# Kernel tuning notes

Measured on AMD Instinct MI355X. Metric: run time of the kernel, lower is better.

## Reference

```python
import jax, jax.numpy as jnp
import numpy as np

DIM = 16
BOND = 4
RANK = 512
N = 50000
E = 400000
F_IN = 16
EDGE_VARIABLE = 2


def setup_inputs() -> dict:
    key = jax.random.key(0)
    ks = iter(jax.random.split(key, 48))
    g = lambda shape, s=0.1: jax.random.normal(next(ks), shape, jnp.float32) * s
    inp = {
        "x": jax.random.normal(next(ks), (N, F_IN), jnp.float32),
        "node_type": jax.random.randint(next(ks), (N,), 0, 3),
        "edge_index": jax.random.randint(next(ks), (2, E), 0, N),
        "edge_attr": jax.random.uniform(next(ks), (E, BOND), dtype=jnp.float32),
        # lin0
        "W_lin0": g((F_IN, DIM)), "b_lin0": jnp.zeros((DIM,), jnp.float32),
        # NNConv: root weight + edge-conditioned weight MLP (4 -> 32 -> dim*dim)
        "W_root": g((DIM, DIM)), "b_conv": jnp.zeros((DIM,), jnp.float32),
        "W_e1": g((BOND, 32)), "b_e1": jnp.zeros((32,), jnp.float32),
        "W_e2": g((32, DIM * DIM)), "b_e2": jnp.zeros((DIM * DIM,), jnp.float32),
        # GRU (torch gate order r,z,n), weights stored torch-style [3*dim, dim]
        "W_ih": g((3 * DIM, DIM)), "b_ih": jnp.zeros((3 * DIM,), jnp.float32),
        "W_hh": g((3 * DIM, DIM)), "b_hh": jnp.zeros((3 * DIM,), jnp.float32),
        # projections
        "W_lin1": g((DIM, BOND)), "b_lin1": jnp.zeros((BOND,), jnp.float32),
        "W_up": g((BOND, DIM)), "b_up": jnp.zeros((DIM,), jnp.float32),
        "W_down": g((DIM, BOND)), "b_down": jnp.zeros((BOND,), jnp.float32),
        # FGNet low-rank factor modules (rank 512)
        "U_B": g((DIM, RANK)), "V_B": g((RANK, DIM)),
        "U_C": g((DIM, RANK)), "V_C": g((RANK, DIM)),
        "U_A": g((BOND, RANK)), "V_A": g((RANK, BOND)),
        # fusion weights
        "w_node": g((1, DIM)), "W_lin": g((DIM, DIM)), "b_lin": jnp.zeros((DIM,), jnp.float32),
        "w_edge": g((1, BOND)), "W_line": g((BOND, BOND)), "b_line": jnp.zeros((BOND,), jnp.float32),
    }
    return inp


def _forward(x, edge_attr, W_lin0, b_lin0, W_root, b_conv, W_e1, b_e1, W_e2, b_e2,
             W_ih, b_ih, W_hh, b_hh, W_lin1, b_lin1, W_up, b_up, W_down, b_down,
             U_B, V_B, U_C, V_C, U_A, V_A, w_node, W_lin, b_lin, w_edge, W_line, b_line,
             node_type, edge_index):
    src, dst = edge_index[0], edge_index[1]

    def nnconv(out):
        # per-edge weight matrices from edge features (edge-conditioned conv)
        he = jax.nn.relu(edge_attr @ W_e1 + b_e1)
        We = (he @ W_e2 + b_e2).reshape(E, DIM, DIM)          # [E, dim, dim]
        m = jnp.einsum('ed,edk->ek', out[src], We)             # gather-multiply
        agg = jax.ops.segment_sum(m, dst, num_segments=N)      # scatter-add
        deg = jax.ops.segment_sum(jnp.ones((E,), out.dtype), dst, num_segments=N)
        agg = agg / jnp.clip(deg, 1.0)[:, None]                # mean aggregation
        return out @ W_root + b_conv + agg

    def gru(inp, h):
        gi = inp @ W_ih.T + b_ih
        gh = h @ W_hh.T + b_hh
        i_r, i_z, i_n = jnp.split(gi, 3, axis=-1)
        h_r, h_z, h_n = jnp.split(gh, 3, axis=-1)
        r = jax.nn.sigmoid(i_r + h_r)
        z = jax.nn.sigmoid(i_z + h_z)
        n = jnp.tanh(i_n + r * h_n)
        return (1.0 - z) * n + z * h

    out = jax.nn.relu(x @ W_lin0 + b_lin0)                     # [N, dim]
    h = out
    for _ in range(3):
        m = jax.nn.relu(nnconv(out))
        h = gru(m, h)
        out = h

    out_edges = jax.nn.relu(out @ W_lin1 + b_lin1)             # [N, bond]

    # one outer message-passing round (k in range(1))
    ev_mask = (node_type == EDGE_VARIABLE)[:, None]
    out_edges_up = out_edges @ W_up + b_up                     # [N, dim]
    out_combine = jnp.where(ev_mask, out_edges_up, out)        # masked replace

    # factor-B message (low-rank FGNet) -> node-dim message + down-projected edge msg
    msg_B = jax.nn.relu((out_combine @ U_B) @ V_B)             # [N, dim]
    msg_to_edge_B = msg_B @ W_down + b_down                    # [N, bond]

    # factor-C message (low-rank FGNet)
    msg_C = jax.nn.relu((out_combine @ U_C) @ V_C)             # [N, dim]

    # factor-A / valence message on edge-type beliefs
    msg_to_edge_A = jax.nn.relu((out_edges @ U_A) @ V_A)       # [N, bond]

    all_msg = msg_B + msg_C                                    # sum over stacked msgs
    combine_edge_msg = msg_to_edge_A * msg_to_edge_B

    out = out + jax.nn.relu((w_node * all_msg) @ W_lin + b_lin)
    out_edges = out_edges + jax.nn.relu((w_edge * combine_edge_msg) @ W_line + b_line)

    return jax.nn.log_softmax(out_edges, axis=-1)              # [N, bond]


def reference(x, node_type, edge_index, edge_attr, W_lin0, b_lin0, W_root, b_conv,
              W_e1, b_e1, W_e2, b_e2, W_ih, b_ih, W_hh, b_hh, W_lin1, b_lin1,
              W_up, b_up, W_down, b_down, U_B, V_B, U_C, V_C, U_A, V_A,
              w_node, W_lin, b_lin, w_edge, W_line, b_line):
    return _forward(x, edge_attr, W_lin0, b_lin0, W_root, b_conv, W_e1, b_e1, W_e2, b_e2,
                    W_ih, b_ih, W_hh, b_hh, W_lin1, b_lin1, W_up, b_up, W_down, b_down,
                    U_B, V_B, U_C, V_C, U_A, V_A, w_node, W_lin, b_lin, w_edge, W_line, b_line,
                    node_type, edge_index)
```

## Files before the change

kernel.cpp:

```cpp
#include <hip/hip_runtime.h>
#include <hip/hip_bf16.h>
#include <math.h>

#define N_NODES 50000
#define N_EDGES 400000
#define DIM 16
#define BOND 4
#define NCHUNK 25000
#define EDGE_GRID 784
#define E_BLOCKS 1563
#define PRE_BASE (E_BLOCKS - 68)
#define SCAN_TILE 1024
#define SCAN_BLOCKS 49

typedef __attribute__((ext_vector_type(8))) short short8;
typedef __attribute__((ext_vector_type(4))) float f32x4;

__device__ __forceinline__ float bf16_to_f32(unsigned short v) {
  return __uint_as_float(((unsigned int)v) << 16);
}

__global__ __launch_bounds__(256) void setup_kernel(
    const float* __restrict__ x, const float* __restrict__ W_lin0,
    const float* __restrict__ b_lin0, const int* __restrict__ ei,
    const float* __restrict__ U_B, const float* __restrict__ V_B,
    const float* __restrict__ U_A, const float* __restrict__ V_A,
    float* __restrict__ out, int* __restrict__ degI, int* __restrict__ rank,
    float* __restrict__ M_B, float* __restrict__ M_A) {
  __shared__ float sW0[256];
  __shared__ float sb0[16];
  int t = threadIdx.x;
  sW0[t] = W_lin0[t];
  if (t < 16) sb0[t] = b_lin0[t];
  __syncthreads();

  int gid = blockIdx.x * 256 + t;

  if (gid < N_NODES) {
    float xr[16];
#pragma unroll
    for (int d = 0; d < 16; ++d) xr[d] = x[gid * 16 + d];
#pragma unroll
    for (int k = 0; k < 16; ++k) {
      float acc = sb0[k];
#pragma unroll
      for (int d = 0; d < 16; ++d) acc += xr[d] * sW0[d * 16 + k];
      out[gid * 16 + k] = fmaxf(acc, 0.f);
    }
  }

  if (gid < N_EDGES) {
    rank[gid] = atomicAdd(&degI[ei[N_EDGES + gid]], 1);
  }

  if (blockIdx.x >= PRE_BASE) {
    int w = (blockIdx.x - PRE_BASE) * 4 + (t >> 6);
    int lane = t & 63;
    float partial = 0.f;
    if (w < 256) {
      int i = w >> 4, j = w & 15;
#pragma unroll
      for (int r8 = 0; r8 < 8; ++r8) {
        int r = lane + 64 * r8;
        partial += U_B[i * 512 + r] * V_B[r * 16 + j];
      }
    } else if (w < 272) {
      int a = (w - 256) >> 2, b = (w - 256) & 3;
#pragma unroll
      for (int r8 = 0; r8 < 8; ++r8) {
        int r = lane + 64 * r8;
        partial += U_A[a * 512 + r] * V_A[r * 4 + b];
      }
    }
#pragma unroll
    for (int off = 32; off > 0; off >>= 1)
      partial += __shfl_down(partial, off);
    if (lane == 0) {
      if (w < 256) M_B[w] = partial;
      else if (w < 272) M_A[w - 256] = partial;
    }
  }
}

__global__ __launch_bounds__(256) void scan_kernel(
    const int* __restrict__ degI, int* ticket, int* st,
    int* __restrict__ row_off) {
  __shared__ int sdata[256];
  __shared__ int s_tile;
  __shared__ int s_base;
  int t = threadIdx.x;
  if (t == 0) s_tile = atomicAdd(ticket, 1);
  __syncthreads();
  int tile = s_tile;
  int n0 = tile * SCAN_TILE + t * 4;

  int d0 = (n0 + 0 < N_NODES) ? degI[n0 + 0] : 0;
  int d1 = (n0 + 1 < N_NODES) ? degI[n0 + 1] : 0;
  int d2 = (n0 + 2 < N_NODES) ? degI[n0 + 2] : 0;
  int d3 = (n0 + 3 < N_NODES) ? degI[n0 + 3] : 0;
  int tsum = d0 + d1 + d2 + d3;
  sdata[t] = tsum;
  __syncthreads();
  for (int off = 1; off < 256; off <<= 1) {
    int v = (t >= off) ? sdata[t - off] : 0;
    __syncthreads();
    sdata[t] += v;
    __syncthreads();
  }
  int excl = sdata[t] - tsum;
  int agg = sdata[255];

  if (t == 0) {
    if (tile == 0) {
      atomicExch(&st[0], (agg << 2) | 2);
      s_base = 0;
    } else {
      atomicExch(&st[tile], (agg << 2) | 1);
      int run = 0, idx = tile - 1;
      while (true) {
        int w = atomicAdd(&st[idx], 0);
        int stt = w & 3;
        if (stt == 2) { run += (w >> 2); break; }
        if (stt == 1) { run += (w >> 2); --idx; }
      }
      atomicExch(&st[tile], ((run + agg) << 2) | 2);
      s_base = run;
    }
  }
  __syncthreads();

  int pre = s_base + excl;
  if (n0 + 0 < N_NODES) row_off[n0 + 0] = pre;
  pre += d0;
  if (n0 + 1 < N_NODES) row_off[n0 + 1] = pre;
  pre += d1;
  if (n0 + 2 < N_NODES) row_off[n0 + 2] = pre;
  pre += d2;
  if (n0 + 3 < N_NODES) row_off[n0 + 3] = pre;
  if (tile == SCAN_BLOCKS - 1 && t == 0) row_off[N_NODES] = N_EDGES;
}

__global__ __launch_bounds__(256) void slot_kernel(
    const int* __restrict__ ei, const int* __restrict__ row_off,
    const int* __restrict__ rank, int* __restrict__ slot) {
  int e = blockIdx.x * 256 + threadIdx.x;
  if (e < N_EDGES) slot[e] = row_off[ei[N_EDGES + e]] + rank[e];
}

__global__ __launch_bounds__(256) void edge_msg_mfma_kernel(
    const int* __restrict__ ei, const float* __restrict__ ea,
    const float* __restrict__ We1, const float* __restrict__ be1,
    const float* __restrict__ We2, const float* __restrict__ be2,
    const float* __restrict__ out, const int* __restrict__ slot,
    unsigned short* __restrict__ m_bufh) {
  __shared__ float sW1T[128];
  __shared__ float sbe1[32];
  int t = threadIdx.x;
  if (t < 128) sW1T[t] = We1[(t & 3) * 32 + 2 * ((t >> 2) & 15) + (t >> 6)];
  if (t < 32) sbe1[t] = be1[2 * (t & 15) + (t >> 4)];

  const int lane = t & 63;
  const int q = lane >> 4, n = lane & 15;
  const int p = q >> 1, dbase = (q & 1) * 8;

  short8 bfrag[17];
#pragma unroll
  for (int s = 0; s < 16; ++s) {
    int h = 2 * s + p;
    union { short8 v; __hip_bfloat162 b2[4]; } bf;
#pragma unroll
    for (int jj = 0; jj < 4; ++jj) {
      float2 w;
      w.x = We2[h * 256 + (dbase + 2 * jj) * 16 + n];
      w.y = We2[h * 256 + (dbase + 2 * jj + 1) * 16 + n];
      bf.b2[jj] = __float22bfloat162_rn(w);
    }
    bfrag[s] = bf.v;
  }
  {
    union { short8 v; __hip_bfloat162 b2[4]; } bf;
#pragma unroll
    for (int jj = 0; jj < 4; ++jj) {
      float2 w;
      if (q < 2) {
        w.x = be2[(dbase + 2 * jj) * 16 + n];
        w.y = be2[(dbase + 2 * jj + 1) * 16 + n];
      } else {
        w.x = 0.f; w.y = 0.f;
      }
      bf.b2[jj] = __float22bfloat162_rn(w);
    }
    bfrag[16] = bf.v;
  }
  __syncthreads();

  const int wave = blockIdx.x * 4 + (t >> 6);
  const int nw = EDGE_GRID * 4;

  int srcP = 0, srcQ = 0;
  float4 avP = {0.f, 0.f, 0.f, 0.f}, avQ = {0.f, 0.f, 0.f, 0.f};
  int4 slP = {0, 0, 0, 0}, slQ = {0, 0, 0, 0};
  float4 oP0 = {0.f, 0.f, 0.f, 0.f}, oP1 = {0.f, 0.f, 0.f, 0.f};

  if (wave < NCHUNK) {
    int e = wave * 16 + n;
    srcP = ei[e];
    avP = ((const float4*)ea)[e];
    slP = *(const int4*)(slot + wave * 16 + q * 4);
  }
  if (wave + nw < NCHUNK) {
    int e = (wave + nw) * 16 + n;
    srcQ = ei[e];
    avQ = ((const float4*)ea)[e];
    slQ = *(const int4*)(slot + (wave + nw) * 16 + q * 4);
  }
  if (wave < NCHUNK) {
    const float4* op = (const float4*)(out + srcP * 16 + dbase);
    oP0 = op[0];
    oP1 = op[1];
  }

  for (int c = wave; c < NCHUNK; c += nw) {
    int srcN = 0;
    float4 avN = {0.f, 0.f, 0.f, 0.f};
    int4 slN = {0, 0, 0, 0};
    int cn2 = c + 2 * nw;
    if (cn2 < NCHUNK) {
      int e = cn2 * 16 + n;
      srcN = ei[e];
      avN = ((const float4*)ea)[e];
      slN = *(const int4*)(slot + cn2 * 16 + q * 4);
    }
    float4 oQ0 = {0.f, 0.f, 0.f, 0.f}, oQ1 = {0.f, 0.f, 0.f, 0.f};
    if (c + nw < NCHUNK) {
      const float4* op = (const float4*)(out + srcQ * 16 + dbase);
      oQ0 = op[0];
      oQ1 = op[1];
    }

    float o[8] = {oP0.x, oP0.y, oP0.z, oP0.w, oP1.x, oP1.y, oP1.z, oP1.w};
    f32x4 acc = {0.f, 0.f, 0.f, 0.f};
#pragma unroll
    for (int s = 0; s < 16; ++s) {
      float4 wj = *(const float4*)&sW1T[(p * 16 + s) * 4];
      float he_s = fmaxf(sbe1[p * 16 + s] + avP.x * wj.x + avP.y * wj.y +
                             avP.z * wj.z + avP.w * wj.w,
                         0.f);
      union { short8 v; __hip_bfloat162 b2[4]; } af;
#pragma unroll
      for (int jj = 0; jj < 4; ++jj) {
        float2 pr;
        pr.x = he_s * o[2 * jj];
        pr.y = he_s * o[2 * jj + 1];
        af.b2[jj] = __float22bfloat162_rn(pr);
      }
      acc = __builtin_amdgcn_mfma_f32_16x16x32_bf16(af.v, bfrag[s], acc, 0, 0, 0);
    }
    {
      union { short8 v; __hip_bfloat162 b2[4]; } af;
#pragma unroll
      for (int jj = 0; jj < 4; ++jj) {
        float2 pr;
        if (q < 2) { pr.x = o[2 * jj]; pr.y = o[2 * jj + 1]; }
        else { pr.x = 0.f; pr.y = 0.f; }
        af.b2[jj] = __float22bfloat162_rn(pr);
      }
      acc = __builtin_amdgcn_mfma_f32_16x16x32_bf16(af.v, bfrag[16], acc, 0, 0, 0);
    }

    __hip_bfloat16 b0 = __float2bfloat16(acc[0]);
    __hip_bfloat16 b1 = __float2bfloat16(acc[1]);
    __hip_bfloat16 b2 = __float2bfloat16(acc[2]);
    __hip_bfloat16 b3 = __float2bfloat16(acc[3]);
    m_bufh[(size_t)slP.x * 16 + n] = *(unsigned short*)&b0;
    m_bufh[(size_t)slP.y * 16 + n] = *(unsigned short*)&b1;
    m_bufh[(size_t)slP.z * 16 + n] = *(unsigned short*)&b2;
    m_bufh[(size_t)slP.w * 16 + n] = *(unsigned short*)&b3;

    avP = avQ; slP = slQ; oP0 = oQ0; oP1 = oQ1;
    srcQ = srcN; avQ = avN; slQ = slN;
  }
}

__global__ __launch_bounds__(256) void gather_gru_kernel(
    const int* __restrict__ row_off, const unsigned short* __restrict__ m_bufh,
    const float* __restrict__ Wroot, const float* __restrict__ bconv,
    const float* __restrict__ Wih, const float* __restrict__ bih,
    const float* __restrict__ Whh, const float* __restrict__ bhh,
    float* __restrict__ out, int do_final, const int* __restrict__ node_type,
    const float* __restrict__ Wlin1, const float* __restrict__ blin1,
    const float* __restrict__ Wup, const float* __restrict__ bup,
    const float* __restrict__ Wdown, const float* __restrict__ bdown,
    const float* __restrict__ M_B, const float* __restrict__ M_A,
    const float* __restrict__ wedge, const float* __restrict__ Wline,
    const float* __restrict__ bline, float* __restrict__ res) {
  __shared__ float sWr[256];
  __shared__ float sWihT[768];
  __shared__ float sWhhT[768];
  __shared__ float sb[112];
  int t = threadIdx.x;
  int kk = t >> 4, dd = t & 15;
  sWr[t] = Wroot[t];
#pragma unroll
  for (int g = 0; g < 3; ++g) {
    sWihT[g * 256 + dd * 16 + kk] = Wih[g * 256 + t];
    sWhhT[g * 256 + dd * 16 + kk] = Whh[g * 256 + t];
  }
  if (t < 16) sb[t] = bconv[t];
  else if (t < 64) sb[t] = bih[t - 16];
  else if (t < 112) sb[t] = bhh[t - 64];
  __syncthreads();

  int n = blockIdx.x * 16 + (t >> 4);
  int k = t & 15;
  int s0 = row_off[n], s1 = row_off[n + 1];

  float aggk = 0.f;
  int j = s0;
  for (; j + 3 < s1; j += 4) {
    float a0 = bf16_to_f32(m_bufh[(size_t)(j + 0) * 16 + k]);
    float a1 = bf16_to_f32(m_bufh[(size_t)(j + 1) * 16 + k]);
    float a2 = bf16_to_f32(m_bufh[(size_t)(j + 2) * 16 + k]);
    float a3 = bf16_to_f32(m_bufh[(size_t)(j + 3) * 16 + k]);
    aggk += (a0 + a1) + (a2 + a3);
  }
  for (; j < s1; ++j) aggk += bf16_to_f32(m_bufh[(size_t)j * 16 + k]);
  float sc = 1.f / fmaxf((float)(s1 - s0), 1.f);

  float hk = out[n * 16 + k];

  float mk = sb[k] + aggk * sc;
#pragma unroll
  for (int d = 0; d < 16; ++d) mk += __shfl(hk, d, 16) * sWr[d * 16 + k];
  mk = fmaxf(mk, 0.f);

  float gir = sb[16 + k], giz = sb[32 + k], gin = sb[48 + k];
  float ghr = sb[64 + k], ghz = sb[80 + k], ghn = sb[96 + k];
#pragma unroll
  for (int d = 0; d < 16; ++d) {
    float md = __shfl(mk, d, 16);
    float hd = __shfl(hk, d, 16);
    gir += md * sWihT[d * 16 + k];
    giz += md * sWihT[256 + d * 16 + k];
    gin += md * sWihT[512 + d * 16 + k];
    ghr += hd * sWhhT[d * 16 + k];
    ghz += hd * sWhhT[256 + d * 16 + k];
    ghn += hd * sWhhT[512 + d * 16 + k];
  }
  float r = 1.f / (1.f + __expf(-(gir + ghr)));
  float z = 1.f / (1.f + __expf(-(giz + ghz)));
  float xn = gin + r * ghn;
  float ng = 1.f - 2.f / (__expf(2.f * xn) + 1.f);
  float hnew = (1.f - z) * ng + z * hk;

  if (!do_final) {
    out[n * 16 + k] = hnew;
    return;
  }

  float p0 = hnew * Wlin1[k * 4 + 0];
  float p1 = hnew * Wlin1[k * 4 + 1];
  float p2 = hnew * Wlin1[k * 4 + 2];
  float p3 = hnew * Wlin1[k * 4 + 3];
#pragma unroll
  for (int msk = 1; msk < 16; msk <<= 1) {
    p0 += __shfl_xor(p0, msk, 16);
    p1 += __shfl_xor(p1, msk, 16);
    p2 += __shfl_xor(p2, msk, 16);
    p3 += __shfl_xor(p3, msk, 16);
  }
  float oe0 = fmaxf(p0 + blin1[0], 0.f);
  float oe1 = fmaxf(p1 + blin1[1], 0.f);
  float oe2 = fmaxf(p2 + blin1[2], 0.f);
  float oe3 = fmaxf(p3 + blin1[3], 0.f);

  bool ev = (node_type[n] == 2);
  float ock = ev ? (bup[k] + oe0 * Wup[k] + oe1 * Wup[16 + k] +
                    oe2 * Wup[32 + k] + oe3 * Wup[48 + k])
                 : hnew;

  float msgBk = 0.f;
#pragma unroll
  for (int d = 0; d < 16; ++d) msgBk += __shfl(ock, d, 16) * M_B[d * 16 + k];
  msgBk = fmaxf(msgBk, 0.f);

  float q0 = msgBk * Wdown[k * 4 + 0];
  float q1 = msgBk * Wdown[k * 4 + 1];
  float q2 = msgBk * Wdown[k * 4 + 2];
  float q3 = msgBk * Wdown[k * 4 + 3];
#pragma unroll
  for (int msk = 1; msk < 16; msk <<= 1) {
    q0 += __shfl_xor(q0, msk, 16);
    q1 += __shfl_xor(q1, msk, 16);
    q2 += __shfl_xor(q2, msk, 16);
    q3 += __shfl_xor(q3, msk, 16);
  }
  float mtb0 = q0 + bdown[0], mtb1 = q1 + bdown[1];
  float mtb2 = q2 + bdown[2], mtb3 = q3 + bdown[3];

  float mta0 = fmaxf(oe0 * M_A[0] + oe1 * M_A[4] + oe2 * M_A[8] + oe3 * M_A[12], 0.f);
  float mta1 = fmaxf(oe0 * M_A[1] + oe1 * M_A[5] + oe2 * M_A[9] + oe3 * M_A[13], 0.f);
  float mta2 = fmaxf(oe0 * M_A[2] + oe1 * M_A[6] + oe2 * M_A[10] + oe3 * M_A[14], 0.f);
  float mta3 = fmaxf(oe0 * M_A[3] + oe1 * M_A[7] + oe2 * M_A[11] + oe3 * M_A[15], 0.f);

  float c0 = wedge[0] * (mta0 * mtb0);
  float c1 = wedge[1] * (mta1 * mtb1);
  float c2 = wedge[2] * (mta2 * mtb2);
  float c3 = wedge[3] * (mta3 * mtb3);

  float f0 = oe0 + fmaxf(bline[0] + c0 * Wline[0] + c1 * Wline[4] +
                         c2 * Wline[8] + c3 * Wline[12], 0.f);
  float f1 = oe1 + fmaxf(bline[1] + c0 * Wline[1] + c1 * Wline[5] +
                         c2 * Wline[9] + c3 * Wline[13], 0.f);
  float f2 = oe2 + fmaxf(bline[2] + c0 * Wline[2] + c1 * Wline[6] +
                         c2 * Wline[10] + c3 * Wline[14], 0.f);
  float f3 = oe3 + fmaxf(bline[3] + c0 * Wline[3] + c1 * Wline[7] +
                         c2 * Wline[11] + c3 * Wline[15], 0.f);

  float mx = fmaxf(fmaxf(f0, f1), fmaxf(f2, f3));
  float se = __expf(f0 - mx) + __expf(f1 - mx) + __expf(f2 - mx) +
             __expf(f3 - mx);
  float lse = mx + __logf(se);
  if (k < 4) {
    float v = (k == 0) ? f0 : (k == 1) ? f1 : (k == 2) ? f2 : f3;
    res[n * 4 + k] = v - lse;
  }
}

extern "C" void kernel_launch(void* const* d_in, const int* in_sizes, int n_in,
                              void* d_out, int out_size, void* d_ws,
                              size_t ws_size, hipStream_t stream) {
  const float* x       = (const float*)d_in[0];
  const int* node_type = (const int*)d_in[1];
  const int* ei        = (const int*)d_in[2];
  const float* ea      = (const float*)d_in[3];
  const float* W_lin0  = (const float*)d_in[4];
  const float* b_lin0  = (const float*)d_in[5];
  const float* W_root  = (const float*)d_in[6];
  const float* b_conv  = (const float*)d_in[7];
  const float* W_e1    = (const float*)d_in[8];
  const float* b_e1    = (const float*)d_in[9];
  const float* W_e2    = (const float*)d_in[10];
  const float* b_e2    = (const float*)d_in[11];
  const float* W_ih    = (const float*)d_in[12];
  const float* b_ih    = (const float*)d_in[13];
  const float* W_hh    = (const float*)d_in[14];
  const float* b_hh    = (const float*)d_in[15];
  const float* W_lin1  = (const float*)d_in[16];
  const float* b_lin1  = (const float*)d_in[17];
  const float* W_up    = (const float*)d_in[18];
  const float* b_up    = (const float*)d_in[19];
  const float* W_down  = (const float*)d_in[20];
  const float* b_down  = (const float*)d_in[21];
  const float* U_B     = (const float*)d_in[22];
  const float* V_B     = (const float*)d_in[23];
  const float* U_A     = (const float*)d_in[26];
  const float* V_A     = (const float*)d_in[27];
  const float* w_edge  = (const float*)d_in[31];
  const float* W_line  = (const float*)d_in[32];
  const float* b_line  = (const float*)d_in[33];

  float* ws    = (float*)d_ws;
  float* out   = ws;
  unsigned short* m_bufh = (unsigned short*)(out + N_NODES * 16);
  float* M_B   = (float*)(m_bufh + (size_t)N_EDGES * 16);
  float* M_A   = M_B + 256;
  int* degI    = (int*)(M_A + 16);
  int* ticket  = degI + N_NODES;
  int* st      = ticket + 1;
  int* row_off = st + 63;
  int* rank    = row_off + N_NODES + 1;
  int* slot    = rank + N_EDGES;

  hipMemsetAsync(degI, 0, (N_NODES + 64) * sizeof(int), stream);

  setup_kernel<<<E_BLOCKS, 256, 0, stream>>>(x, W_lin0, b_lin0, ei, U_B, V_B,
                                             U_A, V_A, out, degI, rank, M_B,
                                             M_A);
  scan_kernel<<<SCAN_BLOCKS, 256, 0, stream>>>(degI, ticket, st, row_off);
  slot_kernel<<<E_BLOCKS, 256, 0, stream>>>(ei, row_off, rank, slot);

  for (int it = 0; it < 3; ++it) {
    edge_msg_mfma_kernel<<<EDGE_GRID, 256, 0, stream>>>(
        ei, ea, W_e1, b_e1, W_e2, b_e2, out, slot, m_bufh);
    gather_gru_kernel<<<N_NODES / 16, 256, 0, stream>>>(
        row_off, m_bufh, W_root, b_conv, W_ih, b_ih, W_hh, b_hh, out,
        (it == 2) ? 1 : 0, node_type, W_lin1, b_lin1, W_up, b_up, W_down,
        b_down, M_B, M_A, w_edge, W_line, b_line, (float*)d_out);
  }
}
```

Measured before the change: 324.7 us.

## Deepen edge-kernel prefetch pipeline and split node gather across four lanes

Measured after the change: 425.3 us. 1.31x slower.

```diff
diff --git a/kernel.cpp b/kernel.cpp
--- a/kernel.cpp
+++ b/kernel.cpp
@@ -7,7 +7,7 @@
 #define DIM 16
 #define BOND 4
 #define NCHUNK 25000
-#define EDGE_GRID 784
+#define EDGE_GRID 1024
 #define E_BLOCKS 1563
 #define PRE_BASE (E_BLOCKS - 68)
 #define SCAN_TILE 1024
@@ -197,46 +197,45 @@
   const int wave = blockIdx.x * 4 + (t >> 6);
   const int nw = EDGE_GRID * 4;
 
-  int srcP = 0, srcQ = 0;
+  int src2 = 0;
   float4 avP = {0.f, 0.f, 0.f, 0.f}, avQ = {0.f, 0.f, 0.f, 0.f};
-  int4 slP = {0, 0, 0, 0}, slQ = {0, 0, 0, 0};
   float4 oP0 = {0.f, 0.f, 0.f, 0.f}, oP1 = {0.f, 0.f, 0.f, 0.f};
-
-  if (wave < NCHUNK) {
-    int e = wave * 16 + n;
-    srcP = ei[e];
-    avP = ((const float4*)ea)[e];
-    slP = *(const int4*)(slot + wave * 16 + q * 4);
-  }
-  if (wave + nw < NCHUNK) {
-    int e = (wave + nw) * 16 + n;
-    srcQ = ei[e];
-    avQ = ((const float4*)ea)[e];
-    slQ = *(const int4*)(slot + (wave + nw) * 16 + q * 4);
-  }
-  if (wave < NCHUNK) {
-    const float4* op = (const float4*)(out + srcP * 16 + dbase);
-    oP0 = op[0];
-    oP1 = op[1];
-  }
-
-  for (int c = wave; c < NCHUNK; c += nw) {
-    int srcN = 0;
-    float4 avN = {0.f, 0.f, 0.f, 0.f};
-    int4 slN = {0, 0, 0, 0};
-    int cn2 = c + 2 * nw;
-    if (cn2 < NCHUNK) {
-      int e = cn2 * 16 + n;
-      srcN = ei[e];
-      avN = ((const float4*)ea)[e];
-      slN = *(const int4*)(slot + cn2 * 16 + q * 4);
-    }
-    float4 oQ0 = {0.f, 0.f, 0.f, 0.f}, oQ1 = {0.f, 0.f, 0.f, 0.f};
-    if (c + nw < NCHUNK) {
-      const float4* op = (const float4*)(out + srcQ * 16 + dbase);
+  float4 oQ0 = {0.f, 0.f, 0.f, 0.f}, oQ1 = {0.f, 0.f, 0.f, 0.f};
+  {
+    int src0 = 0, src1 = 0;
+    if (wave < NCHUNK) {
+      src0 = ei[wave * 16 + n];
+      avP = ((const float4*)ea)[wave * 16 + n];
+    }
+    if (wave + nw < NCHUNK) {
+      src1 = ei[(wave + nw) * 16 + n];
+      avQ = ((const float4*)ea)[(wave + nw) * 16 + n];
+    }
+    if (wave + 2 * nw < NCHUNK) src2 = ei[(wave + 2 * nw) * 16 + n];
+    if (wave < NCHUNK) {
+      const float4* op = (const float4*)(out + src0 * 16 + dbase);
+      oP0 = op[0];
+      oP1 = op[1];
+    }
+    if (wave + nw < NCHUNK) {
+      const float4* op = (const float4*)(out + src1 * 16 + dbase);
       oQ0 = op[0];
       oQ1 = op[1];
     }
+  }
+
+  for (int c = wave; c < NCHUNK; c += nw) {
+    int src3 = 0;
+    float4 avN = {0.f, 0.f, 0.f, 0.f};
+    if (c + 3 * nw < NCHUNK) src3 = ei[(c + 3 * nw) * 16 + n];
+    if (c + 2 * nw < NCHUNK) avN = ((const float4*)ea)[(c + 2 * nw) * 16 + n];
+    float4 oR0 = {0.f, 0.f, 0.f, 0.f}, oR1 = {0.f, 0.f, 0.f, 0.f};
+    if (c + 2 * nw < NCHUNK) {
+      const float4* op = (const float4*)(out + src2 * 16 + dbase);
+      oR0 = op[0];
+      oR1 = op[1];
+    }
+    int4 sl = *(const int4*)(slot + c * 16 + q * 4);
 
     float o[8] = {oP0.x, oP0.y, oP0.z, oP0.w, oP1.x, oP1.y, oP1.z, oP1.w};
     f32x4 acc = {0.f, 0.f, 0.f, 0.f};
@@ -272,13 +271,14 @@
     __hip_bfloat16 b1 = __float2bfloat16(acc[1]);
     __hip_bfloat16 b2 = __float2bfloat16(acc[2]);
     __hip_bfloat16 b3 = __float2bfloat16(acc[3]);
-    m_bufh[(size_t)slP.x * 16 + n] = *(unsigned short*)&b0;
-    m_bufh[(size_t)slP.y * 16 + n] = *(unsigned short*)&b1;
-    m_bufh[(size_t)slP.z * 16 + n] = *(unsigned short*)&b2;
-    m_bufh[(size_t)slP.w * 16 + n] = *(unsigned short*)&b3;
-
-    avP = avQ; slP = slQ; oP0 = oQ0; oP1 = oQ1;
-    srcQ = srcN; avQ = avN; slQ = slN;
+    m_bufh[(size_t)sl.x * 16 + n] = *(unsigned short*)&b0;
+    m_bufh[(size_t)sl.y * 16 + n] = *(unsigned short*)&b1;
+    m_bufh[(size_t)sl.z * 16 + n] = *(unsigned short*)&b2;
+    m_bufh[(size_t)sl.w * 16 + n] = *(unsigned short*)&b3;
+
+    oP0 = oQ0; oP1 = oQ1; oQ0 = oR0; oQ1 = oR1;
+    avP = avQ; avQ = avN;
+    src2 = src3;
   }
 }
 
@@ -299,35 +299,40 @@
   __shared__ float sWhhT[768];
   __shared__ float sb[112];
   int t = threadIdx.x;
-  int kk = t >> 4, dd = t & 15;
-  sWr[t] = Wroot[t];
-#pragma unroll
-  for (int g = 0; g < 3; ++g) {
-    sWihT[g * 256 + dd * 16 + kk] = Wih[g * 256 + t];
-    sWhhT[g * 256 + dd * 16 + kk] = Whh[g * 256 + t];
-  }
-  if (t < 16) sb[t] = bconv[t];
-  else if (t < 64) sb[t] = bih[t - 16];
-  else if (t < 112) sb[t] = bhh[t - 64];
-  __syncthreads();
-
-  int n = blockIdx.x * 16 + (t >> 4);
+  {
+    int kk = t >> 4, dd = t & 15;
+    sWr[t] = Wroot[t];
+#pragma unroll
+    for (int g = 0; g < 3; ++g) {
+      sWihT[g * 256 + dd * 16 + kk] = Wih[g * 256 + t];
+      sWhhT[g * 256 + dd * 16 + kk] = Whh[g * 256 + t];
+    }
+    if (t < 16) sb[t] = bconv[t];
+    else if (t < 64) sb[t] = bih[t - 16];
+    else if (t < 112) sb[t] = bhh[t - 64];
+  }
+  __syncthreads();
+
+  int n = blockIdx.x * 4 + (t >> 6);
   int k = t & 15;
+  int jg = (t >> 4) & 3;
   int s0 = row_off[n], s1 = row_off[n + 1];
 
+  float hk = out[n * 16 + k];
+
   float aggk = 0.f;
-  int j = s0;
-  for (; j + 3 < s1; j += 4) {
-    float a0 = bf16_to_f32(m_bufh[(size_t)(j + 0) * 16 + k]);
-    float a1 = bf16_to_f32(m_bufh[(size_t)(j + 1) * 16 + k]);
-    float a2 = bf16_to_f32(m_bufh[(size_t)(j + 2) * 16 + k]);
-    float a3 = bf16_to_f32(m_bufh[(size_t)(j + 3) * 16 + k]);
-    aggk += (a0 + a1) + (a2 + a3);
-  }
-  for (; j < s1; ++j) aggk += bf16_to_f32(m_bufh[(size_t)j * 16 + k]);
+  int j = s0 + jg;
+  for (; j + 4 < s1; j += 8) {
+    float a0 = bf16_to_f32(m_bufh[(size_t)j * 16 + k]);
+    float a1 = bf16_to_f32(m_bufh[(size_t)(j + 4) * 16 + k]);
+    aggk += a0 + a1;
+  }
+  if (j < s1) { aggk += bf16_to_f32(m_bufh[(size_t)j * 16 + k]); j += 4; }
+  if (j < s1) { aggk += bf16_to_f32(m_bufh[(size_t)j * 16 + k]); }
+  aggk += __shfl_xor(aggk, 16);
+  aggk += __shfl_xor(aggk, 32);
+
   float sc = 1.f / fmaxf((float)(s1 - s0), 1.f);
-
-  float hk = out[n * 16 + k];
 
   float mk = sb[k] + aggk * sc;
 #pragma unroll
@@ -354,7 +359,7 @@
   float hnew = (1.f - z) * ng + z * hk;
 
   if (!do_final) {
-    out[n * 16 + k] = hnew;
+    if (jg == 0) out[n * 16 + k] = hnew;
     return;
   }
 
@@ -421,7 +426,7 @@
   float se = __expf(f0 - mx) + __expf(f1 - mx) + __expf(f2 - mx) +
              __expf(f3 - mx);
   float lse = mx + __logf(se);
-  if (k < 4) {
+  if (jg == 0 && k < 4) {
     float v = (k == 0) ? f0 : (k == 1) ? f1 : (k == 2) ? f2 : f3;
     res[n * 4 + k] = v - lse;
   }
@@ -483,7 +488,7 @@
   for (int it = 0; it < 3; ++it) {
     edge_msg_mfma_kernel<<<EDGE_GRID, 256, 0, stream>>>(
         ei, ea, W_e1, b_e1, W_e2, b_e2, out, slot, m_bufh);
-    gather_gru_kernel<<<N_NODES / 16, 256, 0, stream>>>(
+    gather_gru_kernel<<<N_NODES / 4, 256, 0, stream>>>(
         row_off, m_bufh, W_root, b_conv, W_ih, b_ih, W_hh, b_hh, out,
         (it == 2) ? 1 : 0, node_type, W_lin1, b_lin1, W_up, b_up, W_down,
         b_down, M_B, M_A, w_edge, W_line, b_line, (float*)d_out);
```
